# Kernel optimization log

Measured on AMD Instinct MI355X. Metric: run time of the kernel, lower is better.

The kernel has to match this reference:

```python
import jax, jax.numpy as jnp
import numpy as np


def log_g(x):
    # log of g(x) = where(x>=0, x+0.5, sigmoid(x)), computed stably in log space
    return jnp.where(x >= 0, jnp.log(jax.nn.relu(x) + 0.5), -jax.nn.softplus(-x))


def setup_inputs() -> dict:
    key = jax.random.key(0)
    k1, k2 = jax.random.split(key)
    B, S, D = 4, 4096, 1024
    x = jax.random.normal(k1, (B, S, D), dtype=jnp.float32)
    W_hg = jax.random.normal(k2, (2 * D, D), dtype=jnp.float32) * (1.0 / np.sqrt(D))
    return {"x": x, "W_hg": W_hg}


def reference(x, W_hg):
    # x: [B, S, D], W_hg: [2D, D]
    hg = jnp.einsum('bsd,ed->bse', x, W_hg)  # [B, S, 2D]
    hidden, gate = jnp.split(hg, 2, axis=-1)

    log_coeffs = -jax.nn.softplus(gate)       # log(1 - z)
    log_z = -jax.nn.softplus(-gate)            # log(z)
    log_values = log_z + log_g(hidden)

    # Heinsen associative scan in log space along seq axis
    a_star = jnp.cumsum(log_coeffs, axis=1)
    log_h0_plus_b_star = jax.lax.cumlogsumexp(log_values - a_star, axis=1)
    log_h = a_star + log_h0_plus_b_star
    out = jnp.exp(log_h)  # [B, S, D]; to_out is Identity (expansion_factor=1.0)
    return out
```

## Files before the change

kernel.cpp:

```cpp
#include <hip/hip_runtime.h>
#include <stdint.h>

#define B_ 4
#define S_ 4096
#define D_ 1024
#define E_ 2048
#define K_ 1024
#define M_ (B_*S_)
#define NCHAIN 32
#define SENT 0xFFFFFFFFFFFFFFFFull

typedef __bf16 bf16x8 __attribute__((ext_vector_type(8)));
typedef float  f32x4  __attribute__((ext_vector_type(4)));
typedef _Float16 f16x2 __attribute__((ext_vector_type(2)));

#define BM 128
#define BN 128
#define BK 32

__device__ __forceinline__ unsigned short f2bf(float f) {
    union { float f; unsigned int u; } x; x.f = f;
    unsigned int u = x.u;
    return (unsigned short)((u + 0x7fffu + ((u >> 16) & 1u)) >> 16);
}

__device__ __forceinline__ void gload16(const void* g, void* l) {
    __builtin_amdgcn_global_load_lds(
        (const __attribute__((address_space(1))) void*)(uintptr_t)g,
        (__attribute__((address_space(3))) void*)(uintptr_t)l,
        16, 0, 0);
}

__device__ __forceinline__ unsigned int packCV(float hid, float gat) {
    float e  = __expf(gat);
    float c  = __builtin_amdgcn_rcpf(1.f + e);
    float gg = (hid >= 0.f) ? (hid + 0.5f)
                            : __builtin_amdgcn_rcpf(1.f + __expf(-hid));
    float v  = (1.f - c) * gg;
    union { f16x2 h; unsigned int u; } pk;
    pk.h[0] = (_Float16)c; pk.h[1] = (_Float16)v;
    return pk.u;
}

__global__ __launch_bounds__(256)
void cvt_xw(const float* __restrict__ x, unsigned short* __restrict__ xb,
            const float* __restrict__ w, unsigned short* __restrict__ wb,
            unsigned long long* __restrict__ segAgg) {
    const int b = blockIdx.x;
    const int t = threadIdx.x;
    if (b < 2048) {
        const float4* xp = (const float4*)x + (size_t)b * 2048 + t;
        ushort4*      op = (ushort4*)xb + (size_t)b * 2048 + t;
        float4 f[8];
#pragma unroll
        for (int k = 0; k < 8; k++) f[k] = xp[(size_t)k * 256];
#pragma unroll
        for (int k = 0; k < 8; k++) {
            ushort4 o;
            o.x = f2bf(f[k].x); o.y = f2bf(f[k].y);
            o.z = f2bf(f[k].z); o.w = f2bf(f[k].w);
            op[(size_t)k * 256] = o;
        }
    } else if (b < 2304) {
        const int base4 = (b - 2048) * 2048 + t;
        float4 f[8];
        const float* srcs[8];
#pragma unroll
        for (int k = 0; k < 8; k++) {
            int i = (base4 + k * 256) * 4;
            int r = i >> 10;
            int kk = i & 1023;
            int d = r >> 1, g = r & 1;
            srcs[k] = w + (size_t)(g * D_ + d) * K_ + kk;
        }
#pragma unroll
        for (int k = 0; k < 8; k++) f[k] = *(const float4*)srcs[k];
#pragma unroll
        for (int k = 0; k < 8; k++) {
            int i = (base4 + k * 256) * 4;
            ushort4 o;
            o.x = f2bf(f[k].x); o.y = f2bf(f[k].y);
            o.z = f2bf(f[k].z); o.w = f2bf(f[k].w);
            *(ushort4*)(wb + i) = o;
        }
    } else {
        const size_t base = (size_t)(b - 2304) * 2048 + t;
#pragma unroll
        for (int k = 0; k < 8; k++) segAgg[base + (size_t)k * 256] = SENT;
    }
}

__device__ __forceinline__ void kstep(const unsigned short* Ab, const unsigned short* Bb,
                                      int waveM, int waveN, int mrow, int kg,
                                      f32x4 acc[4][4]) {
    bf16x8 af[4], bfr[4];
#pragma unroll
    for (int i = 0; i < 4; i++)
        af[i] = *(const bf16x8*)(Ab + (size_t)(waveM + i * 16 + mrow) * BK + kg);
#pragma unroll
    for (int j = 0; j < 4; j++)
        bfr[j] = *(const bf16x8*)(Bb + (size_t)(waveN + j * 16 + mrow) * BK + kg);
#pragma unroll
    for (int i = 0; i < 4; i++)
#pragma unroll
        for (int j = 0; j < 4; j++)
            acc[i][j] = __builtin_amdgcn_mfma_f32_16x16x32_bf16(af[i], bfr[j], acc[i][j], 0, 0, 0);
}

__global__ __launch_bounds__(256, 3)
void gemm_fused(const unsigned short* __restrict__ xb,
                const unsigned short* __restrict__ wb,
                unsigned long long* __restrict__ segAgg,
                float* __restrict__ out) {
    __shared__ __align__(16) char smem[39424];
    unsigned short* A0 = (unsigned short*)(smem);
    unsigned short* A1 = (unsigned short*)(smem + 8192);
    unsigned short* Bc0 = (unsigned short*)(smem + 16384);
    unsigned short* Bc1 = (unsigned short*)(smem + 24576);
    unsigned int*   EpBase = (unsigned int*)(smem);
    float* scratch = (float*)(smem + 36864);
    float* hpre    = (float*)(smem + 38912);

    const int ord   = blockIdx.x;
    const int inner = ord & 63;
    const int eB    = inner >> 2;
    const int bat   = inner & 3;
    const int sIx   = ord >> 6;
    const int mB    = bat * NCHAIN + sIx;
    const int mBase = mB * BM;
    const int eBase = eB * BN;

    const int tid  = threadIdx.x;
    const int lane = tid & 63;
    const int w    = tid >> 6;
    const int waveM = (w >> 1) * 64;
    const int waveN = (w & 1) * 64;

    f32x4 acc[4][4] = {};

    const int row0 = tid >> 2, cu = tid & 3;
    const unsigned short* aG0 = xb + (size_t)(mBase + row0) * K_ + cu * 8;
    const unsigned short* aG1 = aG0 + (size_t)64 * K_;
    const unsigned short* bG0 = wb + (size_t)(eBase + row0) * K_ + cu * 8;
    const unsigned short* bG1 = bG0 + (size_t)64 * K_;
    const int woff = w * 512;

    const int mrow = lane & 15;
    const int kg   = (lane >> 4) * 8;

#define STAGE(Ab, Bb, kk) do { \
        gload16(aG0 + (kk), (Ab) + woff); \
        gload16(aG1 + (kk), (Ab) + 2048 + woff); \
        gload16(bG0 + (kk), (Bb) + woff); \
        gload16(bG1 + (kk), (Bb) + 2048 + woff); \
    } while (0)

    STAGE(A0, Bc0, 0);
    __syncthreads();

    for (int k0 = 0; k0 < K_; k0 += 2 * BK) {
        STAGE(A1, Bc1, k0 + BK);
        __builtin_amdgcn_sched_barrier(0);
        kstep(A0, Bc0, waveM, waveN, mrow, kg, acc);
        __syncthreads();
        if (k0 + 2 * BK < K_) {
            STAGE(A0, Bc0, k0 + 2 * BK);
            __builtin_amdgcn_sched_barrier(0);
        }
        kstep(A1, Bc1, waveM, waveN, mrow, kg, acc);
        __syncthreads();
    }
#undef STAGE

    const int q    = lane >> 4;
    const int odd  = lane & 1;
    const int colL = (lane & 15) >> 1;
    unsigned int* EpW = EpBase + w * (64 * 36);

#pragma unroll
    for (int i = 0; i < 4; i++) {
#pragma unroll
        for (int j = 0; j < 4; j++) {
            float o0 = __shfl_xor(acc[i][j][0], 1, 64);
            float o1 = __shfl_xor(acc[i][j][1], 1, 64);
            float o2 = __shfl_xor(acc[i][j][2], 1, 64);
            float o3 = __shfl_xor(acc[i][j][3], 1, 64);
            float m0 = odd ? acc[i][j][2] : acc[i][j][0];
            float m1 = odd ? acc[i][j][3] : acc[i][j][1];
            float p0 = odd ? o2 : o0;
            float p1 = odd ? o3 : o1;
            float h0 = odd ? p0 : m0, g0 = odd ? m0 : p0;
            float h1 = odd ? p1 : m1, g1 = odd ? m1 : p1;
            int row = i * 16 + q * 4 + odd * 2;
            int col = j * 8 + colL;
            EpW[(row    ) * 36 + col] = packCV(h0, g0);
            EpW[(row + 1) * 36 + col] = packCV(h1, g1);
        }
    }

    __syncthreads();

    const int dl = tid & 63;
    const int qt = tid >> 6;
    const int wq = (qt >> 1) * 2 + (dl >> 5);
    const int rB = (qt & 1) * 32;
    const int cc_ = dl & 31;
    const unsigned int* src = EpBase + ((size_t)wq * 64 + rB) * 36 + cc_;
    {
        float C = 1.f, V = 0.f;
#pragma unroll 8
        for (int rr = 0; rr < 32; rr++) {
            union { unsigned int u; f16x2 h; } uu;
            uu.u = src[rr * 36];
            float cv_c = (float)uu.h[0], cv_v = (float)uu.h[1];
            V = fmaf(cv_c, V, cv_v);
            C *= cv_c;
        }
        scratch[(qt * 64 + dl) * 2 + 0] = C;
        scratch[(qt * 64 + dl) * 2 + 1] = V;
    }
    __syncthreads();

    if (tid < 64) {
        float C0 = scratch[(0 * 64 + tid) * 2], V0 = scratch[(0 * 64 + tid) * 2 + 1];
        float C1 = scratch[(1 * 64 + tid) * 2], V1 = scratch[(1 * 64 + tid) * 2 + 1];
        float C2 = scratch[(2 * 64 + tid) * 2], V2 = scratch[(2 * 64 + tid) * 2 + 1];
        float C3 = scratch[(3 * 64 + tid) * 2], V3 = scratch[(3 * 64 + tid) * 2 + 1];
        float Cb = (C0 * C1) * (C2 * C3);
        float Vb = fmaf(C3, fmaf(C2, fmaf(C1, V0, V1), V2), V3);
        union { unsigned long long u; float f[2]; } pk;
        pk.f[0] = Cb; pk.f[1] = Vb;
        __hip_atomic_store(&segAgg[(size_t)ord * 64 + tid], pk.u,
                           __ATOMIC_RELAXED, __HIP_MEMORY_SCOPE_AGENT);

        float h = 0.f;
        const size_t chanB = (size_t)inner * 64 + tid;
#pragma unroll 1
        for (int t0 = 0; t0 < NCHAIN; t0 += 8) {
            if (t0 >= sIx) break;
            unsigned long long vb[8];
#pragma unroll
            for (int k = 0; k < 8; k++)
                vb[k] = (t0 + k < sIx)
                    ? __hip_atomic_load(&segAgg[(size_t)(t0 + k) * 4096 + chanB],
                                        __ATOMIC_RELAXED, __HIP_MEMORY_SCOPE_AGENT)
                    : 0x3f800000ull;
#pragma unroll
            for (int k = 0; k < 8; k++) {
                if (t0 + k < sIx) {
                    while (vb[k] == SENT)
                        vb[k] = __hip_atomic_load(&segAgg[(size_t)(t0 + k) * 4096 + chanB],
                                                  __ATOMIC_RELAXED, __HIP_MEMORY_SCOPE_AGENT);
                }
            }
#pragma unroll
            for (int k = 0; k < 8; k++) {
                union { unsigned long long u; float f[2]; } qd; qd.u = vb[k];
                h = fmaf(qd.f[0], h, qd.f[1]);
            }
        }
        hpre[tid] = h;
    }
    __syncthreads();

    {
        float h = hpre[dl];
        if (qt > 0) h = fmaf(scratch[(0 * 64 + dl) * 2], h, scratch[(0 * 64 + dl) * 2 + 1]);
        if (qt > 1) h = fmaf(scratch[(1 * 64 + dl) * 2], h, scratch[(1 * 64 + dl) * 2 + 1]);
        if (qt > 2) h = fmaf(scratch[(2 * 64 + dl) * 2], h, scratch[(2 * 64 + dl) * 2 + 1]);
        float* outp = out + (size_t)(mBase + qt * 32) * D_ + (eB * 64 + dl);
#pragma unroll 8
        for (int rr = 0; rr < 32; rr++) {
            union { unsigned int u; f16x2 hh; } uu;
            uu.u = src[rr * 36];
            h = fmaf((float)uu.hh[0], h, (float)uu.hh[1]);
            __builtin_nontemporal_store(h, outp + (size_t)rr * D_);
        }
    }
}

extern "C" void kernel_launch(void* const* d_in, const int* in_sizes, int n_in,
                              void* d_out, int out_size, void* d_ws, size_t ws_size,
                              hipStream_t stream) {
    const float* x = (const float*)d_in[0];
    const float* wmat = (const float*)d_in[1];
    float* out = (float*)d_out;
    char* ws = (char*)d_ws;

    unsigned short* xb = (unsigned short*)(ws);
    unsigned short* wb = (unsigned short*)(ws + (32u << 20));
    unsigned long long* segAgg = (unsigned long long*)(ws + (36u << 20));

    cvt_xw<<<2368, 256, 0, stream>>>(x, xb, wmat, wb, segAgg);
    gemm_fused<<<2048, 256, 0, stream>>>(xb, wb, segAgg, out);
}
```

Baseline: 203.1 us.

## Triple-buffer GEMM LDS stages with XOR swizzle and partial vmcnt waits

```diff
diff --git a/kernel.cpp b/kernel.cpp
--- a/kernel.cpp
+++ b/kernel.cpp
@@ -91,15 +91,15 @@
 }
 
 __device__ __forceinline__ void kstep(const unsigned short* Ab, const unsigned short* Bb,
-                                      int waveM, int waveN, int mrow, int kg,
+                                      int waveM, int waveN, int mrow, int kgx,
                                       f32x4 acc[4][4]) {
     bf16x8 af[4], bfr[4];
 #pragma unroll
     for (int i = 0; i < 4; i++)
-        af[i] = *(const bf16x8*)(Ab + (size_t)(waveM + i * 16 + mrow) * BK + kg);
+        af[i] = *(const bf16x8*)(Ab + (size_t)(waveM + i * 16 + mrow) * BK + kgx);
 #pragma unroll
     for (int j = 0; j < 4; j++)
-        bfr[j] = *(const bf16x8*)(Bb + (size_t)(waveN + j * 16 + mrow) * BK + kg);
+        bfr[j] = *(const bf16x8*)(Bb + (size_t)(waveN + j * 16 + mrow) * BK + kgx);
 #pragma unroll
     for (int i = 0; i < 4; i++)
 #pragma unroll
@@ -112,14 +112,16 @@
                 const unsigned short* __restrict__ wb,
                 unsigned long long* __restrict__ segAgg,
                 float* __restrict__ out) {
-    __shared__ __align__(16) char smem[39424];
+    __shared__ __align__(16) char smem[51456];
     unsigned short* A0 = (unsigned short*)(smem);
     unsigned short* A1 = (unsigned short*)(smem + 8192);
-    unsigned short* Bc0 = (unsigned short*)(smem + 16384);
-    unsigned short* Bc1 = (unsigned short*)(smem + 24576);
+    unsigned short* A2 = (unsigned short*)(smem + 16384);
+    unsigned short* B0 = (unsigned short*)(smem + 24576);
+    unsigned short* B1 = (unsigned short*)(smem + 32768);
+    unsigned short* B2 = (unsigned short*)(smem + 40960);
     unsigned int*   EpBase = (unsigned int*)(smem);
-    float* scratch = (float*)(smem + 36864);
-    float* hpre    = (float*)(smem + 38912);
+    float* scratch = (float*)(smem + 49152);
+    float* hpre    = (float*)(smem + 51200);
 
     const int ord   = blockIdx.x;
     const int inner = ord & 63;
@@ -139,14 +141,15 @@
     f32x4 acc[4][4] = {};
 
     const int row0 = tid >> 2, cu = tid & 3;
-    const unsigned short* aG0 = xb + (size_t)(mBase + row0) * K_ + cu * 8;
+    const int cg   = cu ^ ((row0 >> 1) & 3);
+    const unsigned short* aG0 = xb + (size_t)(mBase + row0) * K_ + cg * 8;
     const unsigned short* aG1 = aG0 + (size_t)64 * K_;
-    const unsigned short* bG0 = wb + (size_t)(eBase + row0) * K_ + cu * 8;
+    const unsigned short* bG0 = wb + (size_t)(eBase + row0) * K_ + cg * 8;
     const unsigned short* bG1 = bG0 + (size_t)64 * K_;
     const int woff = w * 512;
 
     const int mrow = lane & 15;
-    const int kg   = (lane >> 4) * 8;
+    const int kgx  = (((lane >> 4) ^ ((mrow >> 1) & 3))) * 8;
 
 #define STAGE(Ab, Bb, kk) do { \
         gload16(aG0 + (kk), (Ab) + woff); \
@@ -155,21 +158,32 @@
         gload16(bG1 + (kk), (Bb) + 2048 + woff); \
     } while (0)
 
-    STAGE(A0, Bc0, 0);
-    __syncthreads();
-
-    for (int k0 = 0; k0 < K_; k0 += 2 * BK) {
-        STAGE(A1, Bc1, k0 + BK);
-        __builtin_amdgcn_sched_barrier(0);
-        kstep(A0, Bc0, waveM, waveN, mrow, kg, acc);
-        __syncthreads();
-        if (k0 + 2 * BK < K_) {
-            STAGE(A0, Bc0, k0 + 2 * BK);
-            __builtin_amdgcn_sched_barrier(0);
-        }
-        kstep(A1, Bc1, waveM, waveN, mrow, kg, acc);
-        __syncthreads();
-    }
+#define STEP_MID(CA, CB, SA, SB, kks) do { \
+        STAGE(SA, SB, (kks)); \
+        __builtin_amdgcn_sched_barrier(0); \
+        kstep(CA, CB, waveM, waveN, mrow, kgx, acc); \
+        asm volatile("s_waitcnt vmcnt(4) lgkmcnt(0)" ::: "memory"); \
+        __builtin_amdgcn_s_barrier(); \
+    } while (0)
+
+    STAGE(A0, B0, 0);
+    STAGE(A1, B1, BK);
+    asm volatile("s_waitcnt vmcnt(4)" ::: "memory");
+    __builtin_amdgcn_s_barrier();
+
+    for (int t = 0; t < 30; t += 3) {
+        const int kk = t * BK;
+        STEP_MID(A0, B0, A2, B2, kk + 2 * BK);
+        STEP_MID(A1, B1, A0, B0, kk + 3 * BK);
+        STEP_MID(A2, B2, A1, B1, kk + 4 * BK);
+    }
+    kstep(A0, B0, waveM, waveN, mrow, kgx, acc);
+    asm volatile("s_waitcnt vmcnt(0) lgkmcnt(0)" ::: "memory");
+    __builtin_amdgcn_s_barrier();
+    kstep(A1, B1, waveM, waveN, mrow, kgx, acc);
+    asm volatile("s_waitcnt lgkmcnt(0)" ::: "memory");
+    __builtin_amdgcn_s_barrier();
+#undef STEP_MID
 #undef STAGE
 
     const int q    = lane >> 4;
```

Result: faster. 198.5 us (-2.2%).
